# Performance work log

Measured on AMD Instinct MI355X. Metric: run time of the kernel, lower is better.

## Reference

```python
import jax, jax.numpy as jnp
import numpy as np

B, H, W, C = 4, 256, 256, 32
K = 5  # per-pixel kernel spatial size (K*K = 25 taps)


def setup_inputs() -> dict:
    key = jax.random.key(0)
    k1, k2, k3 = jax.random.split(key, 3)
    feat = jax.random.normal(k1, (B, H, W, C), dtype=jnp.float32)
    kernel = jax.random.normal(k2, (B, H, W, K * K), dtype=jnp.float32)
    bias = jax.random.normal(k3, (C,), dtype=jnp.float32)
    return {"feat": feat, "kernel": kernel, "bias": bias}


def reference(feat, kernel, bias):
    # Per-pixel predicted convolution (kernel prediction network style):
    # out[b,h,w,c] = sum_{i,j} feat[b, h+i-p, w+j-p, c] * kernel[b,h,w, i*K+j]
    # Kernel taps are shared across channels; SAME zero padding.
    b, h, w, c = feat.shape
    kk = kernel.shape[-1]
    k = int(round(np.sqrt(kk)))
    pad = k // 2
    fp = jnp.pad(feat, ((0, 0), (pad, pad), (pad, pad), (0, 0)))
    out = jnp.zeros_like(feat)
    for i in range(k):          # small fixed K*K loop; avoids materializing
        for j in range(k):      # the [B,H,W,K*K,C] patch tensor
            tap = kernel[..., i * k + j][..., None]          # [B,H,W,1]
            out = out + fp[:, i:i + h, j:j + w, :] * tap      # [B,H,W,C]
    return out + bias  # tf.nn.bias_add, channels_last
```

## Files before the change

kernel.cpp:

```cpp
#include <hip/hip_runtime.h>


#define BB 4
#define HH 256
#define WW 256
#define CC 32
#define KK 5
#define VH 8
#define TW 32
#define TPB 256
#define TROWS (VH + KK - 1)
#define TCOLS (TW + KK - 1)
#define SF_F4 (TROWS * TCOLS * CC / 4)
#define SK_F4 (VH * TW * KK * KK / 4)
#define NQF (SF_F4 / 64)
#define NQ  ((SF_F4 + SK_F4) / 64)

typedef __attribute__((address_space(1))) const void gvoid_t;
typedef __attribute__((address_space(3))) void svoid_t;
typedef float vfloat4 __attribute__((ext_vector_type(4)));

__global__ __launch_bounds__(TPB, 2) void kpn_conv_kernel(
    const float* __restrict__ feat,
    const float* __restrict__ kern,
    const float* __restrict__ bias,
    float* __restrict__ out)
{
    __shared__ float4 sb[SF_F4 + SK_F4];

    const int t    = threadIdx.x;
    const int lane = t & 63;
    const int wave = t >> 6;

    const int bw = blockIdx.x & 7;
    const int bh = (blockIdx.x >> 3) & 31;
    const int b  = blockIdx.x >> 8;
    const int h0 = bh * VH;
    const int w0 = bw * TW;

    const float* fb = feat + (((size_t)b) << 16) * CC;
    const float* kb = kern + (size_t)((b * HH + h0) * WW + w0) * (KK * KK);

    for (int q = wave; q < NQ; q += TPB / 64) {
        if (q < NQF) {
            int e   = (q << 6) + lane;
            int row = e / (TCOLS * CC / 4);
            int rem = e - row * (TCOLS * CC / 4);
            int col = rem >> 3;
            int c4  = rem & 7;
            int hc  = min(max(h0 + row - (KK / 2), 0), HH - 1);
            int wc  = min(max(w0 + col - (KK / 2), 0), WW - 1);
            const float* gp = fb + ((((size_t)hc << 8) + wc) << 5) + (c4 << 2);
            __builtin_amdgcn_global_load_lds((gvoid_t*)gp,
                                             (svoid_t*)(sb + (q << 6)),
                                             16, 0, 0);
        } else {
            int e   = ((q - NQF) << 6) + lane;
            int oh  = e / 200;
            int off = (e - oh * 200) << 2;
            const float* gp = kb + (size_t)oh * (WW * KK * KK) + off;
            __builtin_amdgcn_global_load_lds((gvoid_t*)gp,
                                             (svoid_t*)(sb + SF_F4 + ((q - NQF) << 6)),
                                             16, 0, 0);
        }
    }
    __syncthreads();

    const bool wlo = (w0 == 0), whi = (w0 == WW - TW);
    if (h0 == 0 || h0 == HH - VH || wlo || whi) {
        const float4 z = make_float4(0.f, 0.f, 0.f, 0.f);
        #pragma unroll
        for (int r = 0; r < TROWS; ++r) {
            int hraw = h0 + r - (KK / 2);
            if (hraw < 0 || hraw >= HH) {
                for (int s = t; s < TCOLS * CC / 4; s += TPB)
                    sb[r * (TCOLS * CC / 4) + s] = z;
            }
        }
        if (wlo && t < 192) {
            int r = t >> 4, c = (t >> 3) & 1, c4 = t & 7;
            sb[r * (TCOLS * CC / 4) + c * 8 + c4] = z;
        }
        if (whi && t < 192) {
            int r = t >> 4, c = (TCOLS - 2) + ((t >> 3) & 1), c4 = t & 7;
            sb[r * (TCOLS * CC / 4) + c * 8 + c4] = z;
        }
        __syncthreads();
    }

    const int cg = (t & 7) << 2;
    const int wL = t >> 3;
    const float* sf  = (const float*)sb;
    const float* skw = (const float*)(sb + SF_F4);

    const float4 bz = *(const float4*)(bias + cg);
    float4 acc[VH];
    #pragma unroll
    for (int oh = 0; oh < VH; ++oh) acc[oh] = bz;

    #pragma unroll
    for (int r = 0; r < TROWS; ++r) {
        float4 f[KK];
        #pragma unroll
        for (int j = 0; j < KK; ++j)
            f[j] = *(const float4*)(sf + (r * TCOLS + wL + j) * CC + cg);

        #pragma unroll
        for (int oh = 0; oh < VH; ++oh) {
            const int i = r - oh;
            if (i >= 0 && i < KK) {
                const float* wp = skw + (oh * TW + wL) * (KK * KK) + i * KK;
                const float wg0 = wp[0], wg1 = wp[1], wg2 = wp[2],
                            wg3 = wp[3], wg4 = wp[4];
                acc[oh].x += f[0].x*wg0 + f[1].x*wg1 + f[2].x*wg2 + f[3].x*wg3 + f[4].x*wg4;
                acc[oh].y += f[0].y*wg0 + f[1].y*wg1 + f[2].y*wg2 + f[3].y*wg3 + f[4].y*wg4;
                acc[oh].z += f[0].z*wg0 + f[1].z*wg1 + f[2].z*wg2 + f[3].z*wg3 + f[4].z*wg4;
                acc[oh].w += f[0].w*wg0 + f[1].w*wg1 + f[2].w*wg2 + f[3].w*wg3 + f[4].w*wg4;
            }
        }
    }

    #pragma unroll
    for (int oh = 0; oh < VH; ++oh) {
        const size_t pix = (size_t)(b * HH + h0 + oh) * WW + (w0 + wL);
        vfloat4 v = { acc[oh].x, acc[oh].y, acc[oh].z, acc[oh].w };
        __builtin_nontemporal_store(v, (vfloat4*)(out + pix * CC + cg));
    }
}

extern "C" void kernel_launch(void* const* d_in, const int* in_sizes, int n_in,
                              void* d_out, int out_size, void* d_ws, size_t ws_size,
                              hipStream_t stream) {
    const float* feat = (const float*)d_in[0];
    const float* kern = (const float*)d_in[1];
    const float* bias = (const float*)d_in[2];
    float* out = (float*)d_out;

    dim3 grid(BB * (HH / VH) * (WW / TW));
    dim3 block(TPB);
    kpn_conv_kernel<<<grid, block, 0, stream>>>(feat, kern, bias, out);
}
```

Baseline: 105.1 us.

## Read features directly from global memory and zero boundary taps in kernel weights

Stops staging the feature halo tile in LDS. Feature rows are now loaded straight from global memory with clamped indices, double-buffered in registers and software-pipelined against the FMAs. Padding is handled by zeroing the matching kernel weights in LDS instead of zeroing feature entries. The smaller LDS footprint lets the launch bound ask for 4 blocks per CU. The trade-off is relying on L1/L2 for the repeated feature reads across overlapping rows and columns, plus higher register pressure from the two buffers.

```diff
diff --git a/kernel.cpp b/kernel.cpp
--- a/kernel.cpp
+++ b/kernel.cpp
@@ -10,23 +10,20 @@
 #define TW 32
 #define TPB 256
 #define TROWS (VH + KK - 1)
-#define TCOLS (TW + KK - 1)
-#define SF_F4 (TROWS * TCOLS * CC / 4)
 #define SK_F4 (VH * TW * KK * KK / 4)
-#define NQF (SF_F4 / 64)
-#define NQ  ((SF_F4 + SK_F4) / 64)
+#define NQK (SK_F4 / 64)
 
 typedef __attribute__((address_space(1))) const void gvoid_t;
 typedef __attribute__((address_space(3))) void svoid_t;
 typedef float vfloat4 __attribute__((ext_vector_type(4)));
 
-__global__ __launch_bounds__(TPB, 2) void kpn_conv_kernel(
+__global__ __launch_bounds__(TPB, 4) void kpn_conv_kernel(
     const float* __restrict__ feat,
     const float* __restrict__ kern,
     const float* __restrict__ bias,
     float* __restrict__ out)
 {
-    __shared__ float4 sb[SF_F4 + SK_F4];
+    __shared__ float4 sb[SK_F4];
 
     const int t    = threadIdx.x;
     const int lane = t & 63;
@@ -41,84 +38,107 @@
     const float* fb = feat + (((size_t)b) << 16) * CC;
     const float* kb = kern + (size_t)((b * HH + h0) * WW + w0) * (KK * KK);
 
-    for (int q = wave; q < NQ; q += TPB / 64) {
-        if (q < NQF) {
-            int e   = (q << 6) + lane;
-            int row = e / (TCOLS * CC / 4);
-            int rem = e - row * (TCOLS * CC / 4);
-            int col = rem >> 3;
-            int c4  = rem & 7;
-            int hc  = min(max(h0 + row - (KK / 2), 0), HH - 1);
-            int wc  = min(max(w0 + col - (KK / 2), 0), WW - 1);
-            const float* gp = fb + ((((size_t)hc << 8) + wc) << 5) + (c4 << 2);
-            __builtin_amdgcn_global_load_lds((gvoid_t*)gp,
-                                             (svoid_t*)(sb + (q << 6)),
-                                             16, 0, 0);
-        } else {
-            int e   = ((q - NQF) << 6) + lane;
-            int oh  = e / 200;
-            int off = (e - oh * 200) << 2;
-            const float* gp = kb + (size_t)oh * (WW * KK * KK) + off;
-            __builtin_amdgcn_global_load_lds((gvoid_t*)gp,
-                                             (svoid_t*)(sb + SF_F4 + ((q - NQF) << 6)),
-                                             16, 0, 0);
-        }
+    for (int q = wave; q < NQK; q += TPB / 64) {
+        int e   = (q << 6) + lane;
+        int oh  = e / 200;
+        int off = (e - oh * 200) << 2;
+        const float* gp = kb + (size_t)oh * (WW * KK * KK) + off;
+        __builtin_amdgcn_global_load_lds((gvoid_t*)gp,
+                                         (svoid_t*)(sb + (q << 6)),
+                                         16, 0, 0);
     }
     __syncthreads();
 
+    float* skw_w = (float*)sb;
     const bool wlo = (w0 == 0), whi = (w0 == WW - TW);
-    if (h0 == 0 || h0 == HH - VH || wlo || whi) {
-        const float4 z = make_float4(0.f, 0.f, 0.f, 0.f);
-        #pragma unroll
-        for (int r = 0; r < TROWS; ++r) {
-            int hraw = h0 + r - (KK / 2);
-            if (hraw < 0 || hraw >= HH) {
-                for (int s = t; s < TCOLS * CC / 4; s += TPB)
-                    sb[r * (TCOLS * CC / 4) + s] = z;
+    const bool top = (h0 == 0), bot = (h0 == HH - VH);
+
+    if (wlo || whi || top || bot) {
+        if (wlo) {
+            for (int s = t; s < VH * 15; s += TPB) {
+                int oh = s / 15, rr = s % 15, i = rr / 3, c = rr % 3;
+                int px = (c == 2) ? 1 : 0, j = (c == 2) ? 0 : c;
+                skw_w[(oh * TW + px) * 25 + i * 5 + j] = 0.f;
             }
         }
-        if (wlo && t < 192) {
-            int r = t >> 4, c = (t >> 3) & 1, c4 = t & 7;
-            sb[r * (TCOLS * CC / 4) + c * 8 + c4] = z;
+        if (whi) {
+            for (int s = t; s < VH * 15; s += TPB) {
+                int oh = s / 15, rr = s % 15, i = rr / 3, c = rr % 3;
+                int px = (c == 2) ? 30 : 31, j = (c == 2) ? 4 : (3 + c);
+                skw_w[(oh * TW + px) * 25 + i * 5 + j] = 0.f;
+            }
         }
-        if (whi && t < 192) {
-            int r = t >> 4, c = (TCOLS - 2) + ((t >> 3) & 1), c4 = t & 7;
-            sb[r * (TCOLS * CC / 4) + c * 8 + c4] = z;
+        if (top) {
+            for (int s = t; s < TW * KK; s += TPB) {
+                int px = s / KK, j = s % KK;
+                skw_w[(0 * TW + px) * 25 + 0 * 5 + j] = 0.f;
+                skw_w[(0 * TW + px) * 25 + 1 * 5 + j] = 0.f;
+                skw_w[(1 * TW + px) * 25 + 0 * 5 + j] = 0.f;
+            }
+        }
+        if (bot) {
+            for (int s = t; s < TW * KK; s += TPB) {
+                int px = s / KK, j = s % KK;
+                skw_w[(6 * TW + px) * 25 + 4 * 5 + j] = 0.f;
+                skw_w[(7 * TW + px) * 25 + 3 * 5 + j] = 0.f;
+                skw_w[(7 * TW + px) * 25 + 4 * 5 + j] = 0.f;
+            }
         }
         __syncthreads();
     }
 
     const int cg = (t & 7) << 2;
     const int wL = t >> 3;
-    const float* sf  = (const float*)sb;
-    const float* skw = (const float*)(sb + SF_F4);
+    const float* skw = (const float*)sb;
+
+    int wofs[KK];
+    #pragma unroll
+    for (int j = 0; j < KK; ++j)
+        wofs[j] = min(max(w0 + wL + j - (KK / 2), 0), WW - 1) * CC + cg;
 
     const float4 bz = *(const float4*)(bias + cg);
     float4 acc[VH];
     #pragma unroll
     for (int oh = 0; oh < VH; ++oh) acc[oh] = bz;
 
-    #pragma unroll
-    for (int r = 0; r < TROWS; ++r) {
-        float4 f[KK];
-        #pragma unroll
-        for (int j = 0; j < KK; ++j)
-            f[j] = *(const float4*)(sf + (r * TCOLS + wL + j) * CC + cg);
+#define LOADROW(F, r) {                                                       \
+        int hc = min(max(h0 + (r) - (KK / 2), 0), HH - 1);                    \
+        const float* rp = fb + (size_t)hc * (WW * CC);                        \
+        _Pragma("unroll")                                                     \
+        for (int j = 0; j < KK; ++j)                                          \
+            F[j] = *(const float4*)(rp + wofs[j]);                            \
+    }
 
-        #pragma unroll
-        for (int oh = 0; oh < VH; ++oh) {
-            const int i = r - oh;
-            if (i >= 0 && i < KK) {
-                const float* wp = skw + (oh * TW + wL) * (KK * KK) + i * KK;
-                const float wg0 = wp[0], wg1 = wp[1], wg2 = wp[2],
-                            wg3 = wp[3], wg4 = wp[4];
-                acc[oh].x += f[0].x*wg0 + f[1].x*wg1 + f[2].x*wg2 + f[3].x*wg3 + f[4].x*wg4;
-                acc[oh].y += f[0].y*wg0 + f[1].y*wg1 + f[2].y*wg2 + f[3].y*wg3 + f[4].y*wg4;
-                acc[oh].z += f[0].z*wg0 + f[1].z*wg1 + f[2].z*wg2 + f[3].z*wg3 + f[4].z*wg4;
-                acc[oh].w += f[0].w*wg0 + f[1].w*wg1 + f[2].w*wg2 + f[3].w*wg3 + f[4].w*wg4;
-            }
-        }
+#define FMAROW(F, r) {                                                        \
+        _Pragma("unroll")                                                     \
+        for (int oh = 0; oh < VH; ++oh) {                                     \
+            const int i = (r) - oh;                                           \
+            if (i >= 0 && i < KK) {                                           \
+                const float* wp = skw + (oh * TW + wL) * (KK * KK) + i * KK;  \
+                const float wg0 = wp[0], wg1 = wp[1], wg2 = wp[2],            \
+                            wg3 = wp[3], wg4 = wp[4];                         \
+                acc[oh].x += F[0].x*wg0 + F[1].x*wg1 + F[2].x*wg2 + F[3].x*wg3 + F[4].x*wg4; \
+                acc[oh].y += F[0].y*wg0 + F[1].y*wg1 + F[2].y*wg2 + F[3].y*wg3 + F[4].y*wg4; \
+                acc[oh].z += F[0].z*wg0 + F[1].z*wg1 + F[2].z*wg2 + F[3].z*wg3 + F[4].z*wg4; \
+                acc[oh].w += F[0].w*wg0 + F[1].w*wg1 + F[2].w*wg2 + F[3].w*wg3 + F[4].w*wg4; \
+            }                                                                 \
+        }                                                                     \
     }
+
+    float4 fA[KK], fB[KK];
+    LOADROW(fA, 0)
+    LOADROW(fB, 1)  FMAROW(fA, 0)
+    LOADROW(fA, 2)  FMAROW(fB, 1)
+    LOADROW(fB, 3)  FMAROW(fA, 2)
+    LOADROW(fA, 4)  FMAROW(fB, 3)
+    LOADROW(fB, 5)  FMAROW(fA, 4)
+    LOADROW(fA, 6)  FMAROW(fB, 5)
+    LOADROW(fB, 7)  FMAROW(fA, 6)
+    LOADROW(fA, 8)  FMAROW(fB, 7)
+    LOADROW(fB, 9)  FMAROW(fA, 8)
+    LOADROW(fA, 10) FMAROW(fB, 9)
+    LOADROW(fB, 11) FMAROW(fA, 10)
+                    FMAROW(fB, 11)
 
     #pragma unroll
     for (int oh = 0; oh < VH; ++oh) {
```

Result: slower. 127.3 us (+21.1%).
